# Kernel optimization log

Hardware: AMD Instinct MI355X
Metric: run time of the kernel (lower is better)

Reference implementation:

```python
import jax, jax.numpy as jnp
import numpy as np

B, C, L = 8, 512, 2048
CK = C // 8  # key/query dim of SAGAN attention


def setup_inputs() -> dict:
    key = jax.random.key(0)
    ks = jax.random.split(key, 4)
    s = 0.02  # init scale for weights
    x = jax.random.normal(ks[0], (B, C, L), dtype=jnp.float32)
    Wf = jax.random.normal(ks[1], (CK, C), dtype=jnp.float32) * s
    Wg = jax.random.normal(ks[2], (CK, C), dtype=jnp.float32) * s
    Wh = jax.random.normal(ks[3], (C, C), dtype=jnp.float32) * s
    bf = jnp.zeros((CK,), dtype=jnp.float32)
    bg = jnp.zeros((CK,), dtype=jnp.float32)
    bh = jnp.zeros((C,), dtype=jnp.float32)
    return {"x": x, "Wf": Wf, "bf": bf, "Wg": Wg, "bg": bg, "Wh": Wh, "bh": bh}


def reference(x, Wf, bf, Wg, bg, Wh, bh):
    # conv1x1 projections == channel-mixing matmuls
    f = jnp.einsum('kc,bcl->bkl', Wf, x) + bf[None, :, None]   # (B, CK, L)
    g = jnp.einsum('kc,bcl->bkl', Wg, x) + bg[None, :, None]   # (B, CK, L)
    h = jnp.einsum('oc,bcl->bol', Wh, x) + bh[None, :, None]   # (B, C, L)
    # att[b, i, j] = sum_k f[b,k,i] * g[b,k,j]  (NOTE: no 1/sqrt(d) scale, as in source)
    att = jnp.einsum('bki,bkj->bij', f, g)                      # (B, L, L)
    att = jax.nn.softmax(att, axis=-1)
    self_att = jnp.einsum('bcj,bij->bci', h, att)               # (B, C, L)
    return self_att + x
```

## Files before the change

kernel.cpp:

```cpp
#include <hip/hip_runtime.h>
#include <math.h>
#include <stdint.h>

#define BATCH 8
#define CH    512
#define SEQ   2048
#define CKDIM 64

typedef __attribute__((ext_vector_type(8))) short bf16x8;
typedef __attribute__((ext_vector_type(4))) float f32x4;

__device__ __forceinline__ unsigned short f2b(float f) {
    union { float f; uint32_t u; } v; v.f = f;
    uint32_t u = v.u;
    u += 0x7fffu + ((u >> 16) & 1u);
    return (unsigned short)(u >> 16);
}

__global__ __launch_bounds__(256) void transpose_cast_kernel(
    const float* __restrict__ x, unsigned short* __restrict__ xt)
{
    __shared__ float t[64][65];
    const int b = blockIdx.z, l0 = blockIdx.x * 64, c0 = blockIdx.y * 64;
    const int tx = threadIdx.x & 63, ty = threadIdx.x >> 6;
    #pragma unroll
    for (int q = 0; q < 16; ++q)
        t[ty + q * 4][tx] = x[((size_t)b * CH + c0 + ty + q * 4) * SEQ + l0 + tx];
    __syncthreads();
    #pragma unroll
    for (int q = 0; q < 16; ++q)
        xt[((size_t)b * SEQ + l0 + ty + q * 4) * CH + c0 + tx] = f2b(t[tx][ty + q * 4]);
}

__global__ __launch_bounds__(256) void castw_kernel(
    const float* __restrict__ Wf, const float* __restrict__ Wg,
    const float* __restrict__ Wh, const float* __restrict__ bf_,
    const float* __restrict__ bg_, unsigned short* __restrict__ Wfgb,
    unsigned short* __restrict__ Whb, float* __restrict__ bias_fg)
{
    const int i = blockIdx.x * 256 + threadIdx.x;
    if (i < 128) bias_fg[i] = (i < 64) ? bf_[i] : bg_[i - 64];
    if (i < 65536) Wfgb[i] = f2b((i < 32768) ? Wf[i] : Wg[i - 32768]);
    if (i < 262144) Whb[i] = f2b(Wh[i]);
}

__device__ __attribute__((always_inline)) inline void gemm_core_nt(
    const unsigned short* __restrict__ A, const int ldA,
    const unsigned short* __restrict__ B, const int ldB,
    const int K,
    unsigned short* __restrict__ ldsA, unsigned short* __restrict__ ldsB,
    f32x4 acc[4][4])
{
    const int tid  = threadIdx.x;
    const int lane = tid & 63;
    const int wm   = tid >> 7;
    const int wn   = (tid >> 6) & 1;
    const int fr   = lane & 15;
    const int hi   = lane >> 4;
    const int xo   = lane & 7;

    int goA[4], goB[4], lo[4];
    #pragma unroll
    for (int it = 0; it < 4; ++it) {
        const int idx = tid + it * 256;
        const int row = idx >> 3;
        const int ch  = idx & 7;
        goA[it] = row * ldA + ch * 8;
        goB[it] = row * ldB + ch * 8;
        lo[it]  = row * 64 + ((ch ^ (row & 7)) * 8);
    }
    int aoff[4], boff[4];
    #pragma unroll
    for (int f = 0; f < 4; ++f) {
        aoff[f] = (wm * 64 + f * 16 + fr) * 64;
        boff[f] = (wn * 64 + f * 16 + fr) * 64;
    }
    const int coff0 = ((0 + hi) ^ xo) * 8;
    const int coff1 = ((4 + hi) ^ xo) * 8;

    uint4 ra[4], rb[4];
    #pragma unroll
    for (int it = 0; it < 4; ++it) {
        ra[it] = *(const uint4*)(A + goA[it]);
        rb[it] = *(const uint4*)(B + goB[it]);
    }

    for (int k0 = 0; k0 < K; k0 += 64) {
        #pragma unroll
        for (int it = 0; it < 4; ++it) {
            *(uint4*)&ldsA[lo[it]] = ra[it];
            *(uint4*)&ldsB[lo[it]] = rb[it];
        }
        __syncthreads();
        if (k0 + 64 < K) {
            #pragma unroll
            for (int it = 0; it < 4; ++it) {
                ra[it] = *(const uint4*)(A + goA[it] + k0 + 64);
                rb[it] = *(const uint4*)(B + goB[it] + k0 + 64);
            }
        }
        #pragma unroll
        for (int kk = 0; kk < 2; ++kk) {
            const int co = kk ? coff1 : coff0;
            bf16x8 af[4], bg[4];
            #pragma unroll
            for (int f = 0; f < 4; ++f) {
                af[f] = *(const bf16x8*)&ldsA[aoff[f] + co];
                bg[f] = *(const bf16x8*)&ldsB[boff[f] + co];
            }
            #pragma unroll
            for (int m = 0; m < 4; ++m)
                #pragma unroll
                for (int n = 0; n < 4; ++n)
                    acc[m][n] = __builtin_amdgcn_mfma_f32_16x16x32_bf16(
                        af[m], bg[n], acc[m][n], 0, 0, 0);
        }
        __syncthreads();
    }
}

__device__ __attribute__((always_inline)) inline void epilogue_store_bf16(
    unsigned short* __restrict__ lds, f32x4 acc[4][4],
    unsigned short* __restrict__ outBase, const int ldOut,
    const float* __restrict__ rowBias, const float* __restrict__ colBias)
{
    const int tid = threadIdx.x;
    const int lane = tid & 63;
    const int wm = tid >> 7, wn = (tid >> 6) & 1;
    const int fr = lane & 15, hi = lane >> 4;
    #pragma unroll
    for (int m = 0; m < 4; ++m) {
        const int m0 = wm * 64 + m * 16 + hi * 4;
        #pragma unroll
        for (int n = 0; n < 4; ++n) {
            const int nn = wn * 64 + n * 16 + fr;
            const float cb = colBias ? colBias[nn] : 0.f;
            #pragma unroll
            for (int e = 0; e < 4; ++e) {
                float v = acc[m][n][e] + cb;
                if (rowBias) v += rowBias[m0 + e];
                lds[(m0 + e) * 128 + nn] = f2b(v);
            }
        }
    }
    __syncthreads();
    #pragma unroll
    for (int q = 0; q < 8; ++q) {
        const int idx = tid + q * 256;
        const int row = idx >> 4, ch = idx & 15;
        *(uint4*)&outBase[(size_t)row * ldOut + ch * 8] =
            *(const uint4*)&lds[row * 128 + ch * 8];
    }
}

__global__ __launch_bounds__(256) void proj_fg_kernel(
    const unsigned short* __restrict__ xt, const unsigned short* __restrict__ Wfg,
    const float* __restrict__ bias_fg, unsigned short* __restrict__ fg_t)
{
    __shared__ unsigned short lds[16384];
    const int b = blockIdx.z, i0 = blockIdx.x * 128;
    const unsigned short* A = xt + ((size_t)b * SEQ + i0) * CH;
    f32x4 acc[4][4];
    const f32x4 z = {0.f, 0.f, 0.f, 0.f};
    #pragma unroll
    for (int m = 0; m < 4; ++m)
        #pragma unroll
        for (int n = 0; n < 4; ++n) acc[m][n] = z;
    gemm_core_nt(A, CH, Wfg, CH, CH, lds, lds + 8192, acc);
    epilogue_store_bf16(lds, acc, fg_t + ((size_t)b * SEQ + i0) * 128, 128,
                        nullptr, bias_fg);
}

__global__ __launch_bounds__(256) void proj_h_kernel(
    const unsigned short* __restrict__ xt, const unsigned short* __restrict__ Whb,
    const float* __restrict__ bh, unsigned short* __restrict__ h_b)
{
    __shared__ unsigned short lds[16384];
    const int b = blockIdx.z, l0 = blockIdx.x * 128, c0 = blockIdx.y * 128;
    const unsigned short* A = Whb + (size_t)c0 * CH;
    const unsigned short* B = xt + ((size_t)b * SEQ + l0) * CH;
    f32x4 acc[4][4];
    const f32x4 z = {0.f, 0.f, 0.f, 0.f};
    #pragma unroll
    for (int m = 0; m < 4; ++m)
        #pragma unroll
        for (int n = 0; n < 4; ++n) acc[m][n] = z;
    gemm_core_nt(A, CH, B, CH, CH, lds, lds + 8192, acc);
    epilogue_store_bf16(lds, acc,
                        h_b + ((size_t)b * CH + c0) * SEQ + l0, SEQ,
                        bh + c0, nullptr);
}

__global__ __launch_bounds__(512) void flash_kernel(
    const unsigned short* __restrict__ fg_t,
    const unsigned short* __restrict__ h_b,
    const float* __restrict__ x,
    float* __restrict__ out)
{
    __shared__ __align__(16) char smem[92160];
    unsigned short* h_lds = (unsigned short*)smem;
    unsigned short* P_lds = (unsigned short*)(smem + 65536);
    float* S_lds = (float*)(smem + 73728);
    float* m_lds = (float*)(smem + 91136);
    float* l_lds = (float*)(smem + 91392);
    float* a_lds = (float*)(smem + 91648);
    float* trans = (float*)smem;

    const int tid  = threadIdx.x;
    const int w    = tid >> 6, lane = tid & 63;
    const int fr   = lane & 15, hi = lane >> 4;
    const int flat = blockIdx.x;
    const int b    = flat & 7;
    const int i0   = (flat >> 3) * 64;
    const int ihalf = w & 1, jq = w >> 1;

    if (tid < 64) { m_lds[tid] = -INFINITY; l_lds[tid] = 0.f; }

    bf16x8 qf[2][2];
    #pragma unroll
    for (int m = 0; m < 2; ++m)
        #pragma unroll
        for (int kk = 0; kk < 2; ++kk)
            qf[m][kk] = *(const bf16x8*)(fg_t +
                ((size_t)b * SEQ + i0 + ihalf * 32 + m * 16 + fr) * 128 +
                kk * 32 + hi * 8);

    bf16x8 greg[2];
    uint4 hreg[8];
    #pragma unroll
    for (int kk = 0; kk < 2; ++kk)
        greg[kk] = *(const bf16x8*)(fg_t +
            ((size_t)b * SEQ + jq * 16 + fr) * 128 + 64 + kk * 32 + hi * 8);
    #pragma unroll
    for (int q = 0; q < 8; ++q) {
        const int id = tid + q * 512, c = id >> 3, ch = id & 7;
        hreg[q] = *(const uint4*)(h_b + ((size_t)b * CH + c) * SEQ + ch * 8);
    }

    f32x4 acc[4][4];
    const f32x4 z = {0.f, 0.f, 0.f, 0.f};
    #pragma unroll
    for (int m = 0; m < 4; ++m)
        #pragma unroll
        for (int n = 0; n < 4; ++n) acc[m][n] = z;
    __syncthreads();

    for (int jt = 0; jt < 32; ++jt) {
        #pragma unroll
        for (int q = 0; q < 8; ++q) {
            const int id = tid + q * 512, c = id >> 3, ch = id & 7;
            *(uint4*)&h_lds[c * 64 + ((ch ^ (c & 7)) * 8)] = hreg[q];
        }
        f32x4 sacc[2] = {z, z};
        #pragma unroll
        for (int kk = 0; kk < 2; ++kk)
            #pragma unroll
            for (int m = 0; m < 2; ++m)
                sacc[m] = __builtin_amdgcn_mfma_f32_16x16x32_bf16(
                    qf[m][kk], greg[kk], sacc[m], 0, 0, 0);
        #pragma unroll
        for (int m = 0; m < 2; ++m)
            #pragma unroll
            for (int e = 0; e < 4; ++e)
                S_lds[(ihalf * 32 + m * 16 + hi * 4 + e) * 68 + jq * 16 + fr] =
                    sacc[m][e];
        __syncthreads();

        #pragma unroll
        for (int rr = 0; rr < 8; ++rr) {
            const int r = w * 8 + rr;
            const float sv = S_lds[r * 68 + lane];
            float tmax = sv;
            #pragma unroll
            for (int off = 32; off > 0; off >>= 1)
                tmax = fmaxf(tmax, __shfl_xor(tmax, off));
            const float mo = m_lds[r];
            const float mn = fmaxf(mo, tmax);
            const float p = __expf(sv - mn);
            float ts = p;
            #pragma unroll
            for (int off = 32; off > 0; off >>= 1)
                ts += __shfl_xor(ts, off);
            if (lane == 0) {
                const float al = __expf(mo - mn);
                l_lds[r] = l_lds[r] * al + ts;
                m_lds[r] = mn;
                a_lds[r] = al;
            }
            P_lds[r * 64 + (((lane >> 3) ^ (r & 7)) << 3) + (lane & 7)] = f2b(p);
        }
        if (jt + 1 < 32) {
            #pragma unroll
            for (int kk = 0; kk < 2; ++kk)
                greg[kk] = *(const bf16x8*)(fg_t +
                    ((size_t)b * SEQ + (jt + 1) * 64 + jq * 16 + fr) * 128 +
                    64 + kk * 32 + hi * 8);
            #pragma unroll
            for (int q = 0; q < 8; ++q) {
                const int id = tid + q * 512, c = id >> 3, ch = id & 7;
                hreg[q] = *(const uint4*)(h_b + ((size_t)b * CH + c) * SEQ +
                                          (jt + 1) * 64 + ch * 8);
            }
        }
        __syncthreads();

        #pragma unroll
        for (int m = 0; m < 4; ++m)
            #pragma unroll
            for (int e = 0; e < 4; ++e) {
                const float al = a_lds[m * 16 + hi * 4 + e];
                #pragma unroll
                for (int n = 0; n < 4; ++n)
                    acc[m][n][e] *= al;
            }
        #pragma unroll
        for (int kk = 0; kk < 2; ++kk) {
            bf16x8 pa[4], hb[4];
            #pragma unroll
            for (int m = 0; m < 4; ++m)
                pa[m] = *(const bf16x8*)&P_lds[(m * 16 + fr) * 64 +
                                               (((kk * 4 + hi) ^ (fr & 7)) << 3)];
            #pragma unroll
            for (int n = 0; n < 4; ++n)
                hb[n] = *(const bf16x8*)&h_lds[(w * 64 + n * 16 + fr) * 64 +
                                               (((kk * 4 + hi) ^ (fr & 7)) << 3)];
            #pragma unroll
            for (int m = 0; m < 4; ++m)
                #pragma unroll
                for (int n = 0; n < 4; ++n)
                    acc[m][n] = __builtin_amdgcn_mfma_f32_16x16x32_bf16(
                        pa[m], hb[n], acc[m][n], 0, 0, 0);
        }
        __syncthreads();
    }

    #pragma unroll
    for (int round = 0; round < 2; ++round) {
        __syncthreads();
        if ((w >> 2) == round) {
            float* T = trans + (w & 3) * 4096;
            #pragma unroll
            for (int m = 0; m < 4; ++m)
                #pragma unroll
                for (int e = 0; e < 4; ++e) {
                    const float inv = 1.f / l_lds[m * 16 + hi * 4 + e];
                    #pragma unroll
                    for (int n = 0; n < 4; ++n)
                        T[(n * 16 + fr) * 64 + (((m * 4 + hi) ^ fr) << 2) + e] =
                            acc[m][n][e] * inv;
                }
        }
        __syncthreads();
        #pragma unroll
        for (int q = 0; q < 8; ++q) {
            const int id = tid + q * 512;
            const int c_rel = id >> 4, ich = id & 15;
            const int slot = c_rel >> 6, c_in = c_rel & 63;
            f32x4 v = *(const f32x4*)(trans + slot * 4096 + c_in * 64 +
                                      ((ich ^ (c_in & 15)) << 2));
            const size_t ga = ((size_t)b * CH + round * 256 + c_rel) * SEQ +
                              i0 + ich * 4;
            f32x4 xv = *(const f32x4*)(x + ga);
            *(f32x4*)(out + ga) = v + xv;
        }
    }
}

extern "C" void kernel_launch(void* const* d_in, const int* in_sizes, int n_in,
                              void* d_out, int out_size, void* d_ws, size_t ws_size,
                              hipStream_t stream)
{
    const float* x   = (const float*)d_in[0];
    const float* Wf  = (const float*)d_in[1];
    const float* bf_ = (const float*)d_in[2];
    const float* Wg  = (const float*)d_in[3];
    const float* bg_ = (const float*)d_in[4];
    const float* Wh  = (const float*)d_in[5];
    const float* bh  = (const float*)d_in[6];
    float* out = (float*)d_out;

    unsigned short* ws = (unsigned short*)d_ws;
    size_t off = 0;
    unsigned short* xt   = ws + off; off += (size_t)BATCH * SEQ * CH;
    unsigned short* Wfgb = ws + off; off += 128 * CH;
    unsigned short* Whb  = ws + off; off += CH * CH;
    unsigned short* fg_t = ws + off; off += (size_t)BATCH * SEQ * 128;
    unsigned short* h_b  = ws + off; off += (size_t)BATCH * CH * SEQ;
    float* bias_fg = (float*)(ws + off);

    transpose_cast_kernel<<<dim3(SEQ / 64, CH / 64, BATCH), 256, 0, stream>>>(x, xt);
    castw_kernel<<<dim3(1024), 256, 0, stream>>>(Wf, Wg, Wh, bf_, bg_, Wfgb, Whb, bias_fg);
    proj_fg_kernel<<<dim3(SEQ / 128, 1, BATCH), 256, 0, stream>>>(xt, Wfgb, bias_fg, fg_t);
    proj_h_kernel<<<dim3(SEQ / 128, CH / 128, BATCH), 256, 0, stream>>>(xt, Whb, bh, h_b);
    flash_kernel<<<dim3((SEQ / 64) * BATCH), 512, 0, stream>>>(fg_t, h_b, x, out);
}
```

Baseline: 443.2 us.

## Split flash attention across channel halves with warp-specialized softmax and h loading

The flash kernel now launches twice as many blocks, each covering 256 output channels instead of 512, which shrinks LDS use from about 92KB to about 41KB and sets launch bounds to allow more blocks per CU. Four waves compute QK^T and the online softmax entirely in registers with running max and sum, removing the S_lds round trip. The other four waves stage h tiles into LDS and prefetch the next tile. Each block recomputes the attention scores for its channel half, doubling QK/softmax work in exchange for higher occupancy and fewer barriers per iteration.

Result: faster. 395.5 us (-10.7%).

```diff
diff --git a/kernel.cpp b/kernel.cpp
--- a/kernel.cpp
+++ b/kernel.cpp
@@ -191,177 +191,180 @@
                         bh + c0, nullptr);
 }
 
-__global__ __launch_bounds__(512) void flash_kernel(
+__global__ __launch_bounds__(512, 4) void flash_kernel(
     const unsigned short* __restrict__ fg_t,
     const unsigned short* __restrict__ h_b,
     const float* __restrict__ x,
     float* __restrict__ out)
 {
-    __shared__ __align__(16) char smem[92160];
+    __shared__ __align__(16) char smem[41472];
     unsigned short* h_lds = (unsigned short*)smem;
-    unsigned short* P_lds = (unsigned short*)(smem + 65536);
-    float* S_lds = (float*)(smem + 73728);
-    float* m_lds = (float*)(smem + 91136);
-    float* l_lds = (float*)(smem + 91392);
-    float* a_lds = (float*)(smem + 91648);
-    float* trans = (float*)smem;
+    unsigned short* P_lds = (unsigned short*)(smem + 32768);
+    float* al_lds = (float*)(smem + 40960);
+    float* il_lds = (float*)(smem + 41216);
+    float* trans  = (float*)smem;
 
     const int tid  = threadIdx.x;
     const int w    = tid >> 6, lane = tid & 63;
     const int fr   = lane & 15, hi = lane >> 4;
     const int flat = blockIdx.x;
-    const int b    = flat & 7;
-    const int i0   = (flat >> 3) * 64;
-    const int ihalf = w & 1, jq = w >> 1;
-
-    if (tid < 64) { m_lds[tid] = -INFINITY; l_lds[tid] = 0.f; }
-
-    bf16x8 qf[2][2];
-    #pragma unroll
-    for (int m = 0; m < 2; ++m)
+    const int b     = flat & 7;
+    const int chalf = (flat >> 3) & 1;
+    const int i0    = (flat >> 4) * 64;
+    const int c_base = chalf * 256;
+
+    const f32x4 z = {0.f, 0.f, 0.f, 0.f};
+    f32x4 acc[2][4];
+    #pragma unroll
+    for (int mc = 0; mc < 2; ++mc)
+        #pragma unroll
+        for (int n = 0; n < 4; ++n) acc[mc][n] = z;
+
+    float m_run = -INFINITY, l_run = 0.f;
+    bf16x8 qf[2];
+    uint4 hreg[8];
+
+    if (w < 4) {
         #pragma unroll
         for (int kk = 0; kk < 2; ++kk)
-            qf[m][kk] = *(const bf16x8*)(fg_t +
-                ((size_t)b * SEQ + i0 + ihalf * 32 + m * 16 + fr) * 128 +
-                kk * 32 + hi * 8);
-
-    bf16x8 greg[2];
-    uint4 hreg[8];
-    #pragma unroll
-    for (int kk = 0; kk < 2; ++kk)
-        greg[kk] = *(const bf16x8*)(fg_t +
-            ((size_t)b * SEQ + jq * 16 + fr) * 128 + 64 + kk * 32 + hi * 8);
-    #pragma unroll
-    for (int q = 0; q < 8; ++q) {
-        const int id = tid + q * 512, c = id >> 3, ch = id & 7;
-        hreg[q] = *(const uint4*)(h_b + ((size_t)b * CH + c) * SEQ + ch * 8);
-    }
-
-    f32x4 acc[4][4];
-    const f32x4 z = {0.f, 0.f, 0.f, 0.f};
-    #pragma unroll
-    for (int m = 0; m < 4; ++m)
-        #pragma unroll
-        for (int n = 0; n < 4; ++n) acc[m][n] = z;
+            qf[kk] = *(const bf16x8*)(fg_t +
+                ((size_t)b * SEQ + i0 + 16 * w + fr) * 128 + kk * 32 + hi * 8);
+    } else {
+        const int lid = tid - 256;
+        #pragma unroll
+        for (int q = 0; q < 8; ++q) {
+            const int id = lid + q * 256, c = id >> 3, ch = id & 7;
+            hreg[q] = *(const uint4*)(h_b +
+                ((size_t)b * CH + c_base + c) * SEQ + ch * 8);
+        }
+    }
+
+    for (int jt = 0; jt < 32; ++jt) {
+        __syncthreads();
+        if (w >= 4) {
+            const int lid = tid - 256;
+            #pragma unroll
+            for (int q = 0; q < 8; ++q) {
+                const int id = lid + q * 256, c = id >> 3, ch = id & 7;
+                *(uint4*)&h_lds[c * 64 + ((ch ^ (c & 7)) * 8)] = hreg[q];
+            }
+            if (jt + 1 < 32) {
+                #pragma unroll
+                for (int q = 0; q < 8; ++q) {
+                    const int id = lid + q * 256, c = id >> 3, ch = id & 7;
+                    hreg[q] = *(const uint4*)(h_b +
+                        ((size_t)b * CH + c_base + c) * SEQ + (jt + 1) * 64 + ch * 8);
+                }
+            }
+        } else {
+            f32x4 sacc[4] = {z, z, z, z};
+            #pragma unroll
+            for (int kk = 0; kk < 2; ++kk)
+                #pragma unroll
+                for (int m = 0; m < 4; ++m) {
+                    bf16x8 ga = *(const bf16x8*)(fg_t +
+                        ((size_t)b * SEQ + jt * 64 + 16 * m + fr) * 128 +
+                        64 + kk * 32 + hi * 8);
+                    sacc[m] = __builtin_amdgcn_mfma_f32_16x16x32_bf16(
+                        ga, qf[kk], sacc[m], 0, 0, 0);
+                }
+            float tmax = -INFINITY;
+            #pragma unroll
+            for (int m = 0; m < 4; ++m)
+                #pragma unroll
+                for (int e = 0; e < 4; ++e)
+                    tmax = fmaxf(tmax, sacc[m][e]);
+            tmax = fmaxf(tmax, __shfl_xor(tmax, 16));
+            tmax = fmaxf(tmax, __shfl_xor(tmax, 32));
+            const float mn = fmaxf(m_run, tmax);
+            const float al = __expf(m_run - mn);
+            float p[4][4];
+            float ts = 0.f;
+            #pragma unroll
+            for (int m = 0; m < 4; ++m)
+                #pragma unroll
+                for (int e = 0; e < 4; ++e) {
+                    p[m][e] = __expf(sacc[m][e] - mn);
+                    ts += p[m][e];
+                }
+            ts += __shfl_xor(ts, 16);
+            ts += __shfl_xor(ts, 32);
+            l_run = l_run * al + ts;
+            m_run = mn;
+            if (hi == 0) al_lds[16 * w + fr] = al;
+            #pragma unroll
+            for (int m = 0; m < 4; ++m) {
+                uint2 val;
+                val.x = (uint32_t)f2b(p[m][0]) | ((uint32_t)f2b(p[m][1]) << 16);
+                val.y = (uint32_t)f2b(p[m][2]) | ((uint32_t)f2b(p[m][3]) << 16);
+                const int chunk = (2 * m + (hi >> 1)) ^ (fr & 7);
+                *(uint2*)&P_lds[(16 * w + fr) * 64 + chunk * 8 + (hi & 1) * 4] = val;
+            }
+        }
+        __syncthreads();
+
+        float alv[4];
+        #pragma unroll
+        for (int n = 0; n < 4; ++n) alv[n] = al_lds[16 * n + fr];
+        #pragma unroll
+        for (int mc = 0; mc < 2; ++mc)
+            #pragma unroll
+            for (int n = 0; n < 4; ++n)
+                #pragma unroll
+                for (int e = 0; e < 4; ++e)
+                    acc[mc][n][e] *= alv[n];
+        #pragma unroll
+        for (int kk = 0; kk < 2; ++kk) {
+            const int co = ((kk * 4 + hi) ^ (fr & 7)) * 8;
+            bf16x8 ha[2], pb[4];
+            #pragma unroll
+            for (int mc = 0; mc < 2; ++mc)
+                ha[mc] = *(const bf16x8*)&h_lds[(w * 32 + 16 * mc + fr) * 64 + co];
+            #pragma unroll
+            for (int n = 0; n < 4; ++n)
+                pb[n] = *(const bf16x8*)&P_lds[(16 * n + fr) * 64 + co];
+            #pragma unroll
+            for (int mc = 0; mc < 2; ++mc)
+                #pragma unroll
+                for (int n = 0; n < 4; ++n)
+                    acc[mc][n] = __builtin_amdgcn_mfma_f32_16x16x32_bf16(
+                        ha[mc], pb[n], acc[mc][n], 0, 0, 0);
+        }
+    }
+
     __syncthreads();
-
-    for (int jt = 0; jt < 32; ++jt) {
-        #pragma unroll
-        for (int q = 0; q < 8; ++q) {
-            const int id = tid + q * 512, c = id >> 3, ch = id & 7;
-            *(uint4*)&h_lds[c * 64 + ((ch ^ (c & 7)) * 8)] = hreg[q];
-        }
-        f32x4 sacc[2] = {z, z};
-        #pragma unroll
-        for (int kk = 0; kk < 2; ++kk)
-            #pragma unroll
-            for (int m = 0; m < 2; ++m)
-                sacc[m] = __builtin_amdgcn_mfma_f32_16x16x32_bf16(
-                    qf[m][kk], greg[kk], sacc[m], 0, 0, 0);
-        #pragma unroll
-        for (int m = 0; m < 2; ++m)
-            #pragma unroll
-            for (int e = 0; e < 4; ++e)
-                S_lds[(ihalf * 32 + m * 16 + hi * 4 + e) * 68 + jq * 16 + fr] =
-                    sacc[m][e];
-        __syncthreads();
-
-        #pragma unroll
-        for (int rr = 0; rr < 8; ++rr) {
-            const int r = w * 8 + rr;
-            const float sv = S_lds[r * 68 + lane];
-            float tmax = sv;
-            #pragma unroll
-            for (int off = 32; off > 0; off >>= 1)
-                tmax = fmaxf(tmax, __shfl_xor(tmax, off));
-            const float mo = m_lds[r];
-            const float mn = fmaxf(mo, tmax);
-            const float p = __expf(sv - mn);
-            float ts = p;
-            #pragma unroll
-            for (int off = 32; off > 0; off >>= 1)
-                ts += __shfl_xor(ts, off);
-            if (lane == 0) {
-                const float al = __expf(mo - mn);
-                l_lds[r] = l_lds[r] * al + ts;
-                m_lds[r] = mn;
-                a_lds[r] = al;
-            }
-            P_lds[r * 64 + (((lane >> 3) ^ (r & 7)) << 3) + (lane & 7)] = f2b(p);
-        }
-        if (jt + 1 < 32) {
-            #pragma unroll
-            for (int kk = 0; kk < 2; ++kk)
-                greg[kk] = *(const bf16x8*)(fg_t +
-                    ((size_t)b * SEQ + (jt + 1) * 64 + jq * 16 + fr) * 128 +
-                    64 + kk * 32 + hi * 8);
-            #pragma unroll
-            for (int q = 0; q < 8; ++q) {
-                const int id = tid + q * 512, c = id >> 3, ch = id & 7;
-                hreg[q] = *(const uint4*)(h_b + ((size_t)b * CH + c) * SEQ +
-                                          (jt + 1) * 64 + ch * 8);
-            }
-        }
-        __syncthreads();
-
-        #pragma unroll
-        for (int m = 0; m < 4; ++m)
-            #pragma unroll
-            for (int e = 0; e < 4; ++e) {
-                const float al = a_lds[m * 16 + hi * 4 + e];
+    if (w < 4 && hi == 0) il_lds[16 * w + fr] = 1.f / l_run;
+    __syncthreads();
+    float ilv[4];
+    #pragma unroll
+    for (int n = 0; n < 4; ++n) ilv[n] = il_lds[16 * n + fr];
+
+    #pragma unroll
+    for (int r = 0; r < 2; ++r) {
+        __syncthreads();
+        if ((w >> 2) == r) {
+            #pragma unroll
+            for (int mc = 0; mc < 2; ++mc)
                 #pragma unroll
                 for (int n = 0; n < 4; ++n)
-                    acc[m][n][e] *= al;
-            }
-        #pragma unroll
-        for (int kk = 0; kk < 2; ++kk) {
-            bf16x8 pa[4], hb[4];
-            #pragma unroll
-            for (int m = 0; m < 4; ++m)
-                pa[m] = *(const bf16x8*)&P_lds[(m * 16 + fr) * 64 +
-                                               (((kk * 4 + hi) ^ (fr & 7)) << 3)];
-            #pragma unroll
-            for (int n = 0; n < 4; ++n)
-                hb[n] = *(const bf16x8*)&h_lds[(w * 64 + n * 16 + fr) * 64 +
-                                               (((kk * 4 + hi) ^ (fr & 7)) << 3)];
-            #pragma unroll
-            for (int m = 0; m < 4; ++m)
-                #pragma unroll
-                for (int n = 0; n < 4; ++n)
-                    acc[m][n] = __builtin_amdgcn_mfma_f32_16x16x32_bf16(
-                        pa[m], hb[n], acc[m][n], 0, 0, 0);
-        }
-        __syncthreads();
-    }
-
-    #pragma unroll
-    for (int round = 0; round < 2; ++round) {
-        __syncthreads();
-        if ((w >> 2) == round) {
-            float* T = trans + (w & 3) * 4096;
-            #pragma unroll
-            for (int m = 0; m < 4; ++m)
-                #pragma unroll
-                for (int e = 0; e < 4; ++e) {
-                    const float inv = 1.f / l_lds[m * 16 + hi * 4 + e];
                     #pragma unroll
-                    for (int n = 0; n < 4; ++n)
-                        T[(n * 16 + fr) * 64 + (((m * 4 + hi) ^ fr) << 2) + e] =
-                            acc[m][n][e] * inv;
-                }
-        }
-        __syncthreads();
-        #pragma unroll
-        for (int q = 0; q < 8; ++q) {
+                    for (int e = 0; e < 4; ++e) {
+                        const int c_rel = (w & 3) * 32 + 16 * mc + hi * 4 + e;
+                        trans[c_rel * 64 + ((16 * n + fr) ^ (hi << 4))] =
+                            acc[mc][n][e] * ilv[n];
+                    }
+        }
+        __syncthreads();
+        #pragma unroll
+        for (int q = 0; q < 4; ++q) {
             const int id = tid + q * 512;
-            const int c_rel = id >> 4, ich = id & 15;
-            const int slot = c_rel >> 6, c_in = c_rel & 63;
-            f32x4 v = *(const f32x4*)(trans + slot * 4096 + c_in * 64 +
-                                      ((ich ^ (c_in & 15)) << 2));
-            const size_t ga = ((size_t)b * CH + round * 256 + c_rel) * SEQ +
+            const int c_r = id >> 4, ich = id & 15;
+            f32x4 v = *(const f32x4*)&trans[c_r * 64 +
+                                            ((ich * 4) ^ (((c_r >> 2) & 3) << 4))];
+            const size_t ga = ((size_t)b * CH + c_base + r * 128 + c_r) * SEQ +
                               i0 + ich * 4;
-            f32x4 xv = *(const f32x4*)(x + ga);
-            *(f32x4*)(out + ga) = v + xv;
+            f32x4 xv = *(const f32x4*)&x[ga];
+            *(f32x4*)&out[ga] = v + xv;
         }
     }
 }
@@ -392,5 +395,5 @@
     castw_kernel<<<dim3(1024), 256, 0, stream>>>(Wf, Wg, Wh, bf_, bg_, Wfgb, Whb, bias_fg);
     proj_fg_kernel<<<dim3(SEQ / 128, 1, BATCH), 256, 0, stream>>>(xt, Wfgb, bias_fg, fg_t);
     proj_h_kernel<<<dim3(SEQ / 128, CH / 128, BATCH), 256, 0, stream>>>(xt, Whb, bh, h_b);
-    flash_kernel<<<dim3((SEQ / 64) * BATCH), 512, 0, stream>>>(fg_t, h_b, x, out);
-}
+    flash_kernel<<<dim3(512), 512, 0, stream>>>(fg_t, h_b, x, out);
+}
```
